# Performance work log

Measured on AMD Instinct MI355X. Metric: run time of the kernel, lower is better.

## Reference

```python
import jax, jax.numpy as jnp
import numpy as np

K_NB = 8             # num_neighbors = prop_kernel**2 - 1 (prop_kernel = 3)
IDX_REF = K_NB // 2  # 4 -> center position of the 3x3 kernel
PROP_TIME = 6
EPS_SCALE = 1e-8
EPS_SUM = 1e-4


def _forward(aff_raw, offset, conf, pred_init, dep, aff_scale_const):
    B, _, H, W = pred_init.shape
    dt = pred_init.dtype
    s = aff_scale_const[0]

    # --- TGASS affinity normalization (NLSPNModel._affinity_normalization) ---
    aff = jnp.tanh(aff_raw) / (s + EPS_SCALE)
    asum = jnp.sum(jnp.abs(aff), axis=1, keepdims=True) + EPS_SUM
    asum = jnp.maximum(asum, 1.0)
    aff = aff / asum

    # --- insert reference neighbor: zero offset, aff_ref = 1 - sum(aff) ---
    off = offset.reshape(B, K_NB, 2, H, W)          # (y, x) per neighbor
    zero = jnp.zeros((B, 1, 2, H, W), dt)
    off9 = jnp.concatenate([off[:, :IDX_REF], zero, off[:, IDX_REF:]], axis=1)   # [B,9,2,H,W]
    aff_ref = 1.0 - jnp.sum(aff, axis=1, keepdims=True)
    aff9 = jnp.concatenate([aff[:, :IDX_REF], aff_ref, aff[:, IDX_REF:]], axis=1)  # [B,9,H,W]

    # --- sampling coords: modulated deform conv 3x3, stride=1, pad=1, dil=1, w=ones ---
    k = jnp.arange(9)
    dy = (k // 3 - 1).astype(dt)[None, :, None, None]
    dx = (k % 3 - 1).astype(dt)[None, :, None, None]
    yy = jnp.arange(H, dtype=dt)[None, None, :, None]
    xx = jnp.arange(W, dtype=dt)[None, None, None, :]
    ys = yy + dy + off9[:, :, 0]                    # [B,9,H,W]
    xs = xx + dx + off9[:, :, 1]
    y0 = jnp.floor(ys)
    x0 = jnp.floor(xs)
    wy = ys - y0
    wx = xs - x0
    y0i = y0.astype(jnp.int32)
    x0i = x0.astype(jnp.int32)

    def corner(ff, yi, xi, w):
        # bilinear corner with zero padding outside the image
        valid = ((yi >= 0) & (yi < H) & (xi >= 0) & (xi < W)).astype(dt)
        idx = jnp.clip(yi, 0, H - 1) * W + jnp.clip(xi, 0, W - 1)
        g = jnp.take_along_axis(ff, idx.reshape(B, -1), axis=1).reshape(B, 9, H, W)
        return g * valid * w

    mask_fix = (dep > 0.0).astype(dt)               # preserve sparse input depth

    def step(feat, _):
        ff = (feat * conf)[:, 0].reshape(B, H * W)  # feat * conf, flattened per batch
        sampled = (corner(ff, y0i,     x0i,     (1 - wy) * (1 - wx))
                   + corner(ff, y0i,     x0i + 1, (1 - wy) * wx)
                   + corner(ff, y0i + 1, x0i,     wy * (1 - wx))
                   + corner(ff, y0i + 1, x0i + 1, wy * wx))
        out = jnp.sum(aff9 * sampled, axis=1, keepdims=True)   # [B,1,H,W]
        out = (1.0 - mask_fix) * out + mask_fix * dep
        return out, None

    feat, _ = jax.lax.scan(step, pred_init, None, length=PROP_TIME)
    return feat


def setup_inputs() -> dict:
    key = jax.random.key(0)
    ks = jax.random.split(key, 6)
    B, H, W = 4, 240, 1216
    aff_raw = jax.random.normal(ks[0], (B, K_NB, H, W), jnp.float32)
    offset = jax.random.normal(ks[1], (B, 2 * K_NB, H, W), jnp.float32)
    conf = jax.random.uniform(ks[2], (B, 1, H, W), jnp.float32)
    pred_init = jax.random.uniform(ks[3], (B, 1, H, W), jnp.float32) * 10.0
    u = jax.random.uniform(ks[4], (B, 1, H, W), jnp.float32)
    d = jax.random.uniform(ks[5], (B, 1, H, W), jnp.float32) * 10.0
    dep = jnp.where(u > 0.95, d, 0.0)
    aff_scale_const = jnp.ones((1,), jnp.float32) * 4.0  # gamma(0.5) * num_neighbors(8)
    return {"aff_raw": aff_raw, "offset": offset, "conf": conf,
            "pred_init": pred_init, "dep": dep, "aff_scale_const": aff_scale_const}


def reference(aff_raw, offset, conf, pred_init, dep, aff_scale_const):
    return _forward(aff_raw, offset, conf, pred_init, dep, aff_scale_const)
```

## Files before the change

### kernel.cpp

```cpp
#include <hip/hip_runtime.h>
#include <stdint.h>

#define HNUM 240
#define WNUM 1216
#define BNUM 4
#define HWN (HNUM * WNUM)
#define NPIX (BNUM * HWN)

#define TR 16
#define TC 64
#define RH 12
#define LR (TR + 2 * RH + 1)
#define LC (TC + 2 * RH + 1)
#define LCP 90
#define LDSN (LR * LCP)
#define PXJ 4
#define TGR (HNUM / TR)
#define TGC (WNUM / TC)
#define NTILE (BNUM * TGR * TGC)

union HCV { uint32_t u; _Float16 h[2]; };

__device__ __forceinline__ float fast_tanh(float x) {
    float ax = fabsf(x);
    float e  = __builtin_amdgcn_exp2f(ax * 2.885390081777927f);
    float t  = 1.0f - 2.0f * __builtin_amdgcn_rcpf(e + 1.0f);
    return copysignf(t, x);
}

__global__ __launch_bounds__(256) void nlspn_step1_lds(
    const float* __restrict__ aff_raw,
    const float* __restrict__ offset,
    const float* __restrict__ conf,
    const float* __restrict__ dep,
    const float* __restrict__ pred,
    const float* __restrict__ scale,
    _Float16* __restrict__ planeOut,
    uint4* __restrict__ tapsA,
    uint4* __restrict__ tapsB,
    uint4* __restrict__ affaux)
{
    __shared__ _Float16 tile[LDSN];

    int bid  = blockIdx.x;
    int b    = bid / (TGR * TGC);
    int rem  = bid - b * (TGR * TGC);
    int tr   = rem / TGC;
    int tc   = rem - tr * TGC;
    int tid  = (int)threadIdx.x;
    int lane = tid & 63;
    int wrow = tid >> 6;

    int row0 = tr * TR - RH;
    int col0 = tc * TC - RH;

    for (int i = tid; i < LDSN; i += 256) {
        int lr = i / LCP;
        int lc = i - lr * LCP;
        int gr = row0 + lr;
        int gc = col0 + lc;
        float v = 0.f;
        if (lc < LC && gr >= 0 && gr < HNUM && gc >= 0 && gc < WNUM) {
            int pi = b * HWN + gr * WNUM + gc;
            v = pred[pi] * conf[pi];
        }
        tile[i] = (_Float16)v;
    }
    __syncthreads();

    float s    = scale[0];
    float invs = 1.0f / (s + 1e-8f);

#pragma unroll
    for (int j = 0; j < PXJ; ++j) {
        int rj = wrow * PXJ + j;
        int h  = tr * TR + rj;
        int w  = tc * TC + lane;
        int hw = h * WNUM + w;
        int p  = b * HWN + hw;

        const float* arb = aff_raw + (size_t)b * 8 * HWN + hw;
        float aa[8];
        float asum = 0.f;
#pragma unroll
        for (int k = 0; k < 8; ++k) {
            float t = fast_tanh(arb[(size_t)k * HWN]) * invs;
            aa[k] = t;
            asum += fabsf(t);
        }
        float rden = 1.0f / fmaxf(asum + 1e-4f, 1.0f);
        float sm = 0.f;
#pragma unroll
        for (int k = 0; k < 8; ++k) { aa[k] *= rden; sm += aa[k]; }
        float aref = 1.0f - sm;

        int cbase = (RH + rj) * LCP + (RH + lane);
        float acc = aref * (float)tile[cbase];

        const float* ofb = offset + (size_t)b * 16 * HWN + hw;
        uint32_t tw[8];
#pragma unroll
        for (int k = 0; k < 8; ++k) {
            int k9 = (k < 4) ? k : k + 1;
            int dy = k9 / 3 - 1;
            int dx = k9 - (k9 / 3) * 3 - 1;
            float offy = ofb[(size_t)(2 * k)     * HWN];
            float offx = ofb[(size_t)(2 * k + 1) * HWN];
            float ys  = (float)(h + dy) + offy;
            float xs  = (float)(w + dx) + offx;
            float y0f = floorf(ys), x0f = floorf(xs);
            float wyf = ys - y0f,   wxf = xs - x0f;
            int drow = (int)y0f - h;
            int dcol = (int)x0f - w;
            uint32_t qy = (uint32_t)(wyf * 255.0f + 0.5f); if (qy > 255) qy = 255;
            uint32_t qx = (uint32_t)(wxf * 255.0f + 0.5f); if (qx > 255) qx = 255;
            int lr = RH + rj + drow;
            int lc = RH + lane + dcol;
            if (lr < 0 || lr > LR - 2 || lc < 0 || lc > LC - 2) {
                drow = 0; dcol = 0; qy = 0; qx = 0; aa[k] = 0.f;
            }
            tw[k] = (uint32_t)(uint8_t)(int8_t)drow
                  | ((uint32_t)(uint8_t)(int8_t)dcol << 8)
                  | (qy << 16) | (qx << 24);

            int la = cbase + drow * LCP + dcol;
            float g00 = (float)tile[la];
            float g01 = (float)tile[la + 1];
            float g10 = (float)tile[la + LCP];
            float g11 = (float)tile[la + LCP + 1];
            float fwy = (float)qy * (1.0f / 255.0f);
            float fwx = (float)qx * (1.0f / 255.0f);
            float top = fmaf(fwx, g01 - g00, g00);
            float bot = fmaf(fwx, g11 - g10, g10);
            acc = fmaf(aa[k], fmaf(fwy, bot - top, top), acc);
        }

        tapsA[p] = make_uint4(tw[0], tw[1], tw[2], tw[3]);
        tapsB[p] = make_uint4(tw[4], tw[5], tw[6], tw[7]);

        uint32_t pk[2] = {0u, 0u};
#pragma unroll
        for (int k = 0; k < 8; ++k) {
            int q = (int)floorf(aa[k] * 127.0f + 0.5f);
            q = (q < -127) ? -127 : ((q > 127) ? 127 : q);
            pk[k >> 2] |= ((uint32_t)(uint8_t)(int8_t)q) << (8 * (k & 3));
        }
        float cf = conf[p];
        float dd = dep[p];
        HCV cv;
        cv.h[0] = (_Float16)aref;
        cv.h[1] = (_Float16)cf;
        affaux[p] = make_uint4(pk[0], pk[1], cv.u, __float_as_uint(dd));

        float feat = (dd > 0.f) ? dd : acc;
        planeOut[p] = (_Float16)(feat * cf);
    }
}

template <bool LAST>
__global__ __launch_bounds__(256) void nlspn_prop_lds(
    const uint4* __restrict__ tapsA,
    const uint4* __restrict__ tapsB,
    const uint4* __restrict__ affaux,
    const _Float16* __restrict__ planeIn,
    _Float16* __restrict__ planeOut,
    float* __restrict__ out)
{
    __shared__ _Float16 tile[LDSN];

    int bid  = blockIdx.x;
    int b    = bid / (TGR * TGC);
    int rem  = bid - b * (TGR * TGC);
    int tr   = rem / TGC;
    int tc   = rem - tr * TGC;
    int tid  = (int)threadIdx.x;
    int lane = tid & 63;
    int wrow = tid >> 6;

    int row0 = tr * TR - RH;
    int col0 = tc * TC - RH;
    const _Float16* pb = planeIn + (size_t)b * HWN;

    for (int i = tid; i < LDSN; i += 256) {
        int lr = i / LCP;
        int lc = i - lr * LCP;
        int gr = row0 + lr;
        int gc = col0 + lc;
        _Float16 v = (_Float16)0.f;
        if (lc < LC && gr >= 0 && gr < HNUM && gc >= 0 && gc < WNUM)
            v = pb[gr * WNUM + gc];
        tile[i] = v;
    }
    __syncthreads();

#pragma unroll
    for (int j = 0; j < PXJ; ++j) {
        int rj = wrow * PXJ + j;
        int h  = tr * TR + rj;
        int w  = tc * TC + lane;
        int p  = b * HWN + h * WNUM + w;

        uint4 tA = tapsA[p];
        uint4 tB = tapsB[p];
        uint4 ax = affaux[p];

        float af[8];
        int32_t vx = (int32_t)ax.x;
        int32_t vy = (int32_t)ax.y;
        af[0] = (float)((vx << 24) >> 24) * (1.0f / 127.0f);
        af[1] = (float)((vx << 16) >> 24) * (1.0f / 127.0f);
        af[2] = (float)((vx <<  8) >> 24) * (1.0f / 127.0f);
        af[3] = (float)( vx        >> 24) * (1.0f / 127.0f);
        af[4] = (float)((vy << 24) >> 24) * (1.0f / 127.0f);
        af[5] = (float)((vy << 16) >> 24) * (1.0f / 127.0f);
        af[6] = (float)((vy <<  8) >> 24) * (1.0f / 127.0f);
        af[7] = (float)( vy        >> 24) * (1.0f / 127.0f);

        HCV cv; cv.u = ax.z;
        float aref = (float)cv.h[0];
        float cf   = (float)cv.h[1];
        float dd   = __uint_as_float(ax.w);

        int cbase = (RH + rj) * LCP + (RH + lane);
        float acc = aref * (float)tile[cbase];

        uint32_t tm[8] = {tA.x, tA.y, tA.z, tA.w, tB.x, tB.y, tB.z, tB.w};
#pragma unroll
        for (int k = 0; k < 8; ++k) {
            uint32_t m = tm[k];
            int drow = (int)(int8_t)(m & 0xffu);
            int dcol = (int)(int8_t)((m >> 8) & 0xffu);
            float wy = (float)((m >> 16) & 0xffu) * (1.0f / 255.0f);
            float wx = (float)(m >> 24)           * (1.0f / 255.0f);
            int la = cbase + drow * LCP + dcol;
            float g00 = (float)tile[la];
            float g01 = (float)tile[la + 1];
            float g10 = (float)tile[la + LCP];
            float g11 = (float)tile[la + LCP + 1];
            float top = fmaf(wx, g01 - g00, g00);
            float bot = fmaf(wx, g11 - g10, g10);
            acc = fmaf(af[k], fmaf(wy, bot - top, top), acc);
        }

        float feat = (dd > 0.f) ? dd : acc;
        if (LAST) out[p] = feat;
        else      planeOut[p] = (_Float16)(feat * cf);
    }
}

__global__ __launch_bounds__(256) void nlspn_init_kernel(
    const float* __restrict__ pred,
    const float* __restrict__ conf,
    float* __restrict__ ff)
{
    int p = blockIdx.x * blockDim.x + threadIdx.x;
    if (p < NPIX) ff[p] = pred[p] * conf[p];
}

template <bool LAST>
__global__ __launch_bounds__(256) void nlspn_prop_kernel(
    const float* __restrict__ aff_raw,
    const float* __restrict__ offset,
    const float* __restrict__ conf,
    const float* __restrict__ dep,
    const float* __restrict__ scale,
    const float* __restrict__ ff_in,
    float* __restrict__ out)
{
    int p = blockIdx.x * blockDim.x + threadIdx.x;
    if (p >= NPIX) return;
    int b  = p / HWN;
    int hw = p - b * HWN;
    int h  = hw / WNUM;
    int w  = hw - h * WNUM;

    float s    = scale[0];
    float invs = 1.0f / (s + 1e-8f);

    float a[8];
    const float* ar = aff_raw + (size_t)b * 8 * HWN + hw;
#pragma unroll
    for (int k = 0; k < 8; ++k) a[k] = ar[(size_t)k * HWN];

    float asum = 0.0f;
#pragma unroll
    for (int k = 0; k < 8; ++k) {
        a[k] = fast_tanh(a[k]) * invs;
        asum += fabsf(a[k]);
    }
    asum += 1e-4f;
    float rden = 1.0f / fmaxf(asum, 1.0f);
    float suma = 0.0f;
#pragma unroll
    for (int k = 0; k < 8; ++k) { a[k] *= rden; suma += a[k]; }
    float aref = 1.0f - suma;

    const float* ffb = ff_in + (size_t)b * HWN;
    float acc = aref * ffb[hw];

    const float* off = offset + (size_t)b * 16 * HWN + hw;
#pragma unroll
    for (int k = 0; k < 8; ++k) {
        int   k9 = (k < 4) ? k : k + 1;
        int   dy = k9 / 3 - 1;
        int   dx = k9 - (k9 / 3) * 3 - 1;
        float offy = off[(size_t)(2 * k)     * HWN];
        float offx = off[(size_t)(2 * k + 1) * HWN];
        float ysf = (float)(h + dy) + offy;
        float xsf = (float)(w + dx) + offx;
        float y0f = floorf(ysf);
        float x0f = floorf(xsf);
        float wy  = ysf - y0f;
        float wx  = xsf - x0f;
        int   y0  = (int)y0f;
        int   x0  = (int)x0f;
        bool yv0 = (y0 >= 0)  & (y0 < HNUM);
        bool yv1 = (y0 >= -1) & (y0 + 1 < HNUM);
        bool xv0 = (x0 >= 0)  & (x0 < WNUM);
        bool xv1 = (x0 >= -1) & (x0 + 1 < WNUM);
        int row0 = y0 * WNUM;
        float g00 = 0.f, g01 = 0.f, g10 = 0.f, g11 = 0.f;
        if (yv0 & xv0) g00 = ffb[row0 + x0];
        if (yv0 & xv1) g01 = ffb[row0 + x0 + 1];
        if (yv1 & xv0) g10 = ffb[row0 + WNUM + x0];
        if (yv1 & xv1) g11 = ffb[row0 + WNUM + x0 + 1];
        float sampled = (1.f - wy) * ((1.f - wx) * g00 + wx * g01)
                      +        wy  * ((1.f - wx) * g10 + wx * g11);
        acc += a[k] * sampled;
    }

    float dd   = dep[p];
    float feat = (dd > 0.0f) ? dd : acc;
    if (LAST) out[p] = feat;
    else      out[p] = feat * conf[p];
}

extern "C" void kernel_launch(void* const* d_in, const int* in_sizes, int n_in,
                              void* d_out, int out_size, void* d_ws, size_t ws_size,
                              hipStream_t stream)
{
    const float* aff_raw = (const float*)d_in[0];
    const float* offset  = (const float*)d_in[1];
    const float* conf    = (const float*)d_in[2];
    const float* pred    = (const float*)d_in[3];
    const float* dep     = (const float*)d_in[4];
    const float* scale   = (const float*)d_in[5];
    float* out = (float*)d_out;

    const int threads = 256;
    const size_t need = (size_t)NPIX * 48 + (size_t)NPIX * 2 * 2 + 64;

    if (ws_size >= need) {
        char* wb = (char*)d_ws;
        uint4* tapsA  = (uint4*)wb;  wb += (size_t)NPIX * 16;
        uint4* tapsB  = (uint4*)wb;  wb += (size_t)NPIX * 16;
        uint4* affaux = (uint4*)wb;  wb += (size_t)NPIX * 16;
        _Float16* plA = (_Float16*)wb;  wb += (size_t)NPIX * 2;
        _Float16* plB = (_Float16*)wb;

        nlspn_step1_lds<<<NTILE, threads, 0, stream>>>(
            aff_raw, offset, conf, dep, pred, scale,
            plB, tapsA, tapsB, affaux);
        nlspn_prop_lds<false><<<NTILE, threads, 0, stream>>>(
            tapsA, tapsB, affaux, plB, plA, out);
        nlspn_prop_lds<false><<<NTILE, threads, 0, stream>>>(
            tapsA, tapsB, affaux, plA, plB, out);
        nlspn_prop_lds<false><<<NTILE, threads, 0, stream>>>(
            tapsA, tapsB, affaux, plB, plA, out);
        nlspn_prop_lds<false><<<NTILE, threads, 0, stream>>>(
            tapsA, tapsB, affaux, plA, plB, out);
        nlspn_prop_lds<true><<<NTILE, threads, 0, stream>>>(
            tapsA, tapsB, affaux, plB, plA, out);
    } else {
        const int blocksP = (NPIX + threads - 1) / threads;
        float* ws = (float*)d_ws;
        nlspn_init_kernel<<<blocksP, threads, 0, stream>>>(pred, conf, out);
        nlspn_prop_kernel<false><<<blocksP, threads, 0, stream>>>(aff_raw, offset, conf, dep, scale, out, ws);
        nlspn_prop_kernel<false><<<blocksP, threads, 0, stream>>>(aff_raw, offset, conf, dep, scale, ws, out);
        nlspn_prop_kernel<false><<<blocksP, threads, 0, stream>>>(aff_raw, offset, conf, dep, scale, out, ws);
        nlspn_prop_kernel<false><<<blocksP, threads, 0, stream>>>(aff_raw, offset, conf, dep, scale, ws, out);
        nlspn_prop_kernel<false><<<blocksP, threads, 0, stream>>>(aff_raw, offset, conf, dep, scale, out, ws);
        nlspn_prop_kernel<true ><<<blocksP, threads, 0, stream>>>(aff_raw, offset, conf, dep, scale, ws, out);
    }
}
```

Before: 121.4 us.

## Split metadata build from propagation and pack affinities into tap words

The first kernel becomes a pure per-pixel metadata builder using float2 vectorized loads. It no longer tiles into LDS or performs the first propagation step, so six propagation launches now run instead of five. Each tap word now packs 4-bit row/col offsets, the 8-bit bilinear weights and the int8 affinity, which shrinks the auxiliary record from 16 to 8 bytes per pixel. The LDS halo is reduced from 12 to 8 to match the 4-bit offset range. This cuts per-pass metadata traffic and LDS footprint, at the cost of an extra full propagation pass and dropping any tap whose offset exceeds the narrower range.

```diff
diff --git a/kernel.cpp b/kernel.cpp
--- a/kernel.cpp
+++ b/kernel.cpp
@@ -6,13 +6,15 @@
 #define BNUM 4
 #define HWN (HNUM * WNUM)
 #define NPIX (BNUM * HWN)
+#define NP2T (NPIX / 2)
+#define GRIDM (NP2T / 256)
 
 #define TR 16
 #define TC 64
-#define RH 12
+#define RH 8
 #define LR (TR + 2 * RH + 1)
 #define LC (TC + 2 * RH + 1)
-#define LCP 90
+#define LCP 82
 #define LDSN (LR * LCP)
 #define PXJ 4
 #define TGR (HNUM / TR)
@@ -28,65 +30,61 @@
     return copysignf(t, x);
 }
 
-__global__ __launch_bounds__(256) void nlspn_step1_lds(
+__global__ __launch_bounds__(256) void nlspn_meta_build(
     const float* __restrict__ aff_raw,
     const float* __restrict__ offset,
     const float* __restrict__ conf,
     const float* __restrict__ dep,
     const float* __restrict__ pred,
     const float* __restrict__ scale,
-    _Float16* __restrict__ planeOut,
+    _Float16* __restrict__ plane0,
     uint4* __restrict__ tapsA,
     uint4* __restrict__ tapsB,
-    uint4* __restrict__ affaux)
-{
-    __shared__ _Float16 tile[LDSN];
-
-    int bid  = blockIdx.x;
-    int b    = bid / (TGR * TGC);
-    int rem  = bid - b * (TGR * TGC);
-    int tr   = rem / TGC;
-    int tc   = rem - tr * TGC;
-    int tid  = (int)threadIdx.x;
-    int lane = tid & 63;
-    int wrow = tid >> 6;
-
-    int row0 = tr * TR - RH;
-    int col0 = tc * TC - RH;
-
-    for (int i = tid; i < LDSN; i += 256) {
-        int lr = i / LCP;
-        int lc = i - lr * LCP;
-        int gr = row0 + lr;
-        int gc = col0 + lc;
-        float v = 0.f;
-        if (lc < LC && gr >= 0 && gr < HNUM && gc >= 0 && gc < WNUM) {
-            int pi = b * HWN + gr * WNUM + gc;
-            v = pred[pi] * conf[pi];
-        }
-        tile[i] = (_Float16)v;
-    }
-    __syncthreads();
+    uint2* __restrict__ auxv)
+{
+    int t = blockIdx.x * 256 + (int)threadIdx.x;
+    int p0 = 2 * t;
+    int b  = p0 / HWN;
+    int hw = p0 - b * HWN;
+    int h  = hw / WNUM;
+    int w0 = hw - h * WNUM;
 
     float s    = scale[0];
     float invs = 1.0f / (s + 1e-8f);
 
-#pragma unroll
-    for (int j = 0; j < PXJ; ++j) {
-        int rj = wrow * PXJ + j;
-        int h  = tr * TR + rj;
-        int w  = tc * TC + lane;
-        int hw = h * WNUM + w;
-        int p  = b * HWN + hw;
-
-        const float* arb = aff_raw + (size_t)b * 8 * HWN + hw;
+    const float* arb = aff_raw + (size_t)b * 8 * HWN + hw;
+    const float* ofb = offset  + (size_t)b * 16 * HWN + hw;
+
+    float2 ar2[8], oy2[8], ox2[8];
+#pragma unroll
+    for (int k = 0; k < 8; ++k)
+        ar2[k] = *(const float2*)(arb + (size_t)k * HWN);
+#pragma unroll
+    for (int k = 0; k < 8; ++k) {
+        oy2[k] = *(const float2*)(ofb + (size_t)(2 * k)     * HWN);
+        ox2[k] = *(const float2*)(ofb + (size_t)(2 * k + 1) * HWN);
+    }
+    float2 cf2 = *(const float2*)(conf + p0);
+    float2 dd2 = *(const float2*)(dep  + p0);
+    float2 pp2 = *(const float2*)(pred + p0);
+
+    _Float16 plo[2];
+
+#pragma unroll
+    for (int jj = 0; jj < 2; ++jj) {
+        int w = w0 + jj;
+        float cf = (jj == 0) ? cf2.x : cf2.y;
+        float dd = (jj == 0) ? dd2.x : dd2.y;
+        float pp = (jj == 0) ? pp2.x : pp2.y;
+
         float aa[8];
         float asum = 0.f;
 #pragma unroll
         for (int k = 0; k < 8; ++k) {
-            float t = fast_tanh(arb[(size_t)k * HWN]) * invs;
-            aa[k] = t;
-            asum += fabsf(t);
+            float rv = (jj == 0) ? ar2[k].x : ar2[k].y;
+            float v  = fast_tanh(rv) * invs;
+            aa[k] = v;
+            asum += fabsf(v);
         }
         float rden = 1.0f / fmaxf(asum + 1e-4f, 1.0f);
         float sm = 0.f;
@@ -94,74 +92,58 @@
         for (int k = 0; k < 8; ++k) { aa[k] *= rden; sm += aa[k]; }
         float aref = 1.0f - sm;
 
-        int cbase = (RH + rj) * LCP + (RH + lane);
-        float acc = aref * (float)tile[cbase];
-
-        const float* ofb = offset + (size_t)b * 16 * HWN + hw;
         uint32_t tw[8];
 #pragma unroll
         for (int k = 0; k < 8; ++k) {
             int k9 = (k < 4) ? k : k + 1;
             int dy = k9 / 3 - 1;
             int dx = k9 - (k9 / 3) * 3 - 1;
-            float offy = ofb[(size_t)(2 * k)     * HWN];
-            float offx = ofb[(size_t)(2 * k + 1) * HWN];
+            float offy = (jj == 0) ? oy2[k].x : oy2[k].y;
+            float offx = (jj == 0) ? ox2[k].x : ox2[k].y;
             float ys  = (float)(h + dy) + offy;
             float xs  = (float)(w + dx) + offx;
             float y0f = floorf(ys), x0f = floorf(xs);
             float wyf = ys - y0f,   wxf = xs - x0f;
-            int drow = (int)y0f - h;
-            int dcol = (int)x0f - w;
+            int y0 = (int)y0f;
+            int x0 = (int)x0f;
+            int drow = y0 - h;
+            int dcol = x0 - w;
             uint32_t qy = (uint32_t)(wyf * 255.0f + 0.5f); if (qy > 255) qy = 255;
             uint32_t qx = (uint32_t)(wxf * 255.0f + 0.5f); if (qx > 255) qx = 255;
-            int lr = RH + rj + drow;
-            int lc = RH + lane + dcol;
-            if (lr < 0 || lr > LR - 2 || lc < 0 || lc > LC - 2) {
-                drow = 0; dcol = 0; qy = 0; qx = 0; aa[k] = 0.f;
-            }
-            tw[k] = (uint32_t)(uint8_t)(int8_t)drow
-                  | ((uint32_t)(uint8_t)(int8_t)dcol << 8)
-                  | (qy << 16) | (qx << 24);
-
-            int la = cbase + drow * LCP + dcol;
-            float g00 = (float)tile[la];
-            float g01 = (float)tile[la + 1];
-            float g10 = (float)tile[la + LCP];
-            float g11 = (float)tile[la + LCP + 1];
-            float fwy = (float)qy * (1.0f / 255.0f);
-            float fwx = (float)qx * (1.0f / 255.0f);
-            float top = fmaf(fwx, g01 - g00, g00);
-            float bot = fmaf(fwx, g11 - g10, g10);
-            acc = fmaf(aa[k], fmaf(fwy, bot - top, top), acc);
+            float av = aa[k];
+            bool ok = (y0 >= -1) & (y0 <= HNUM) & (x0 >= -1) & (x0 <= WNUM)
+                    & (drow >= -8) & (drow <= 7) & (dcol >= -8) & (dcol <= 7);
+            if (!ok) { drow = 0; dcol = 0; qy = 0; qx = 0; av = 0.f; }
+            int q8 = (int)floorf(av * 127.0f + 0.5f);
+            q8 = (q8 < -127) ? -127 : ((q8 > 127) ? 127 : q8);
+            tw[k] = ((uint32_t)drow & 0xfu)
+                  | (((uint32_t)dcol & 0xfu) << 4)
+                  | (qy << 8) | (qx << 16)
+                  | ((uint32_t)(uint8_t)(int8_t)q8 << 24);
         }
 
-        tapsA[p] = make_uint4(tw[0], tw[1], tw[2], tw[3]);
-        tapsB[p] = make_uint4(tw[4], tw[5], tw[6], tw[7]);
-
-        uint32_t pk[2] = {0u, 0u};
-#pragma unroll
-        for (int k = 0; k < 8; ++k) {
-            int q = (int)floorf(aa[k] * 127.0f + 0.5f);
-            q = (q < -127) ? -127 : ((q > 127) ? 127 : q);
-            pk[k >> 2] |= ((uint32_t)(uint8_t)(int8_t)q) << (8 * (k & 3));
-        }
-        float cf = conf[p];
-        float dd = dep[p];
+        tapsA[p0 + jj] = make_uint4(tw[0], tw[1], tw[2], tw[3]);
+        tapsB[p0 + jj] = make_uint4(tw[4], tw[5], tw[6], tw[7]);
+
         HCV cv;
         cv.h[0] = (_Float16)aref;
         cv.h[1] = (_Float16)cf;
-        affaux[p] = make_uint4(pk[0], pk[1], cv.u, __float_as_uint(dd));
-
-        float feat = (dd > 0.f) ? dd : acc;
-        planeOut[p] = (_Float16)(feat * cf);
-    }
+        auxv[p0 + jj] = make_uint2(cv.u, __float_as_uint(dd));
+
+        plo[jj] = (_Float16)(pp * cf);
+    }
+
+    HCV pv;
+    pv.h[0] = plo[0];
+    pv.h[1] = plo[1];
+    *(uint32_t*)(plane0 + p0) = pv.u;
 }
 
 template <bool LAST>
 __global__ __launch_bounds__(256) void nlspn_prop_lds(
     const uint4* __restrict__ tapsA,
     const uint4* __restrict__ tapsB,
-    const uint4* __restrict__ affaux,
+    const uint2* __restrict__ auxv,
     const _Float16* __restrict__ planeIn,
     _Float16* __restrict__ planeOut,
     float* __restrict__ out)
@@ -202,24 +184,12 @@
 
         uint4 tA = tapsA[p];
         uint4 tB = tapsB[p];
-        uint4 ax = affaux[p];
-
-        float af[8];
-        int32_t vx = (int32_t)ax.x;
-        int32_t vy = (int32_t)ax.y;
-        af[0] = (float)((vx << 24) >> 24) * (1.0f / 127.0f);
-        af[1] = (float)((vx << 16) >> 24) * (1.0f / 127.0f);
-        af[2] = (float)((vx <<  8) >> 24) * (1.0f / 127.0f);
-        af[3] = (float)( vx        >> 24) * (1.0f / 127.0f);
-        af[4] = (float)((vy << 24) >> 24) * (1.0f / 127.0f);
-        af[5] = (float)((vy << 16) >> 24) * (1.0f / 127.0f);
-        af[6] = (float)((vy <<  8) >> 24) * (1.0f / 127.0f);
-        af[7] = (float)( vy        >> 24) * (1.0f / 127.0f);
-
-        HCV cv; cv.u = ax.z;
+        uint2 ax = auxv[p];
+
+        HCV cv; cv.u = ax.x;
         float aref = (float)cv.h[0];
         float cf   = (float)cv.h[1];
-        float dd   = __uint_as_float(ax.w);
+        float dd   = __uint_as_float(ax.y);
 
         int cbase = (RH + rj) * LCP + (RH + lane);
         float acc = aref * (float)tile[cbase];
@@ -228,10 +198,11 @@
 #pragma unroll
         for (int k = 0; k < 8; ++k) {
             uint32_t m = tm[k];
-            int drow = (int)(int8_t)(m & 0xffu);
-            int dcol = (int)(int8_t)((m >> 8) & 0xffu);
-            float wy = (float)((m >> 16) & 0xffu) * (1.0f / 255.0f);
-            float wx = (float)(m >> 24)           * (1.0f / 255.0f);
+            int drow = ((int)(m << 28)) >> 28;
+            int dcol = ((int)(m << 24)) >> 28;
+            float wy = (float)((m >> 8)  & 0xffu) * (1.0f / 255.0f);
+            float wx = (float)((m >> 16) & 0xffu) * (1.0f / 255.0f);
+            float af = (float)((int)m >> 24) * (1.0f / 127.0f);
             int la = cbase + drow * LCP + dcol;
             float g00 = (float)tile[la];
             float g01 = (float)tile[la + 1];
@@ -239,7 +210,7 @@
             float g11 = (float)tile[la + LCP + 1];
             float top = fmaf(wx, g01 - g00, g00);
             float bot = fmaf(wx, g11 - g10, g10);
-            acc = fmaf(af[k], fmaf(wy, bot - top, top), acc);
+            acc = fmaf(af, fmaf(wy, bot - top, top), acc);
         }
 
         float feat = (dd > 0.f) ? dd : acc;
@@ -348,29 +319,31 @@
     float* out = (float*)d_out;
 
     const int threads = 256;
-    const size_t need = (size_t)NPIX * 48 + (size_t)NPIX * 2 * 2 + 64;
+    const size_t need = (size_t)NPIX * 44 + 64;
 
     if (ws_size >= need) {
         char* wb = (char*)d_ws;
         uint4* tapsA  = (uint4*)wb;  wb += (size_t)NPIX * 16;
         uint4* tapsB  = (uint4*)wb;  wb += (size_t)NPIX * 16;
-        uint4* affaux = (uint4*)wb;  wb += (size_t)NPIX * 16;
+        uint2* auxv   = (uint2*)wb;  wb += (size_t)NPIX * 8;
         _Float16* plA = (_Float16*)wb;  wb += (size_t)NPIX * 2;
         _Float16* plB = (_Float16*)wb;
 
-        nlspn_step1_lds<<<NTILE, threads, 0, stream>>>(
+        nlspn_meta_build<<<GRIDM, threads, 0, stream>>>(
             aff_raw, offset, conf, dep, pred, scale,
-            plB, tapsA, tapsB, affaux);
-        nlspn_prop_lds<false><<<NTILE, threads, 0, stream>>>(
-            tapsA, tapsB, affaux, plB, plA, out);
-        nlspn_prop_lds<false><<<NTILE, threads, 0, stream>>>(
-            tapsA, tapsB, affaux, plA, plB, out);
-        nlspn_prop_lds<false><<<NTILE, threads, 0, stream>>>(
-            tapsA, tapsB, affaux, plB, plA, out);
-        nlspn_prop_lds<false><<<NTILE, threads, 0, stream>>>(
-            tapsA, tapsB, affaux, plA, plB, out);
+            plA, tapsA, tapsB, auxv);
+        nlspn_prop_lds<false><<<NTILE, threads, 0, stream>>>(
+            tapsA, tapsB, auxv, plA, plB, out);
+        nlspn_prop_lds<false><<<NTILE, threads, 0, stream>>>(
+            tapsA, tapsB, auxv, plB, plA, out);
+        nlspn_prop_lds<false><<<NTILE, threads, 0, stream>>>(
+            tapsA, tapsB, auxv, plA, plB, out);
+        nlspn_prop_lds<false><<<NTILE, threads, 0, stream>>>(
+            tapsA, tapsB, auxv, plB, plA, out);
+        nlspn_prop_lds<false><<<NTILE, threads, 0, stream>>>(
+            tapsA, tapsB, auxv, plA, plB, out);
         nlspn_prop_lds<true><<<NTILE, threads, 0, stream>>>(
-            tapsA, tapsB, affaux, plB, plA, out);
+            tapsA, tapsB, auxv, plB, plA, out);
     } else {
         const int blocksP = (NPIX + threads - 1) / threads;
         float* ws = (float*)d_ws;
```

Result: faster. 112.6 us (median of 3 runs) (-7.2%).
